# Optimization experiments

Measured on AMD Instinct MI355X. Metric: run time of the kernel, lower is better.

## Reference

```python
import jax, jax.numpy as jnp
import numpy as np

B, T, H, L = 256, 1024, 64, 5  # batch, seq_len, hidden_size, num_layers


def setup_inputs() -> dict:
    key = jax.random.key(0)
    ks = jax.random.split(key, 10)
    s = 1.0 / np.sqrt(H)  # PyTorch LSTM/Linear uniform init bound

    def u(k, shape):
        return jax.random.uniform(k, shape, jnp.float32, -s, s)

    return {
        "x": jax.random.normal(ks[0], (B, T, 1), jnp.float32),
        "w_ih0": u(ks[1], (4 * H, 1)),          # layer 0 input weights (input_size=1)
        "w_ih_rest": u(ks[2], (L - 1, 4 * H, H)),  # layers 1..4 input weights
        "w_hh": u(ks[3], (L, 4 * H, H)),
        "b_ih": u(ks[4], (L, 4 * H)),
        "b_hh": u(ks[5], (L, 4 * H)),
        "W1": u(ks[6], (H, H)),
        "b1": u(ks[7], (H,)),
        "W2": u(ks[8], (1, H)),
        "b2": u(ks[9], (1,)),
        "future": 0,
    }


def _lstm_layer(x, w_ih, w_hh, b_ih, b_hh):
    # x: [B, T, in]; PyTorch gate order i, f, g, o
    gx = jnp.einsum('bti,gi->btg', x, w_ih) + b_ih  # precompute input projections [B,T,4H]
    h0 = jnp.zeros((x.shape[0], w_hh.shape[1]), x.dtype)

    def step(carry, gxt):
        h, c = carry
        gates = gxt + h @ w_hh.T + b_hh  # [B,4H]
        i, f, g, o = jnp.split(gates, 4, axis=-1)
        c = jax.nn.sigmoid(f) * c + jax.nn.sigmoid(i) * jnp.tanh(g)
        h = jax.nn.sigmoid(o) * jnp.tanh(c)
        return (h, c), h

    _, hs = jax.lax.scan(step, (h0, h0), jnp.swapaxes(gx, 0, 1))  # scan over time
    return jnp.swapaxes(hs, 0, 1)  # [B,T,H]


def _model(x, w_ih0, w_ih_rest, w_hh, b_ih, b_hh, W1, b1, W2, b2):
    # 5-layer LSTM (inter-layer dropout=0.1 is inactive in eval mode)
    h = _lstm_layer(x, w_ih0, w_hh[0], b_ih[0], b_hh[0])
    for l in range(1, w_hh.shape[0]):
        h = _lstm_layer(h, w_ih_rest[l - 1], w_hh[l], b_ih[l], b_hh[l])
    h = jax.nn.relu(h)
    h = jax.nn.relu(h @ W1.T + b1)
    return h @ W2.T + b2  # [B,T,1]


def reference(x, w_ih0, w_ih_rest, w_hh, b_ih, b_hh, W1, b1, W2, b2, future):
    out = None
    for _ in range(future + 1):
        out = _model(x, w_ih0, w_ih_rest, w_hh, b_ih, b_hh, W1, b1, W2, b2)
        x = jnp.concatenate([x, out[:, -1:, :]], axis=1)
    return out
```

## Files before the change

kernel.cpp:

```cpp
#include <hip/hip_runtime.h>

#define B_ 256
#define T_ 1024
#define H_ 64

typedef float f32x2 __attribute__((ext_vector_type(2)));
typedef float f32x4 __attribute__((ext_vector_type(4)));

__device__ __forceinline__ float fast_sigmoid(float x) {
    float e = __builtin_amdgcn_exp2f(-1.4426950408889634f * x);
    return __builtin_amdgcn_rcpf(1.0f + e);
}
__device__ __forceinline__ float fast_tanh(float x) {
    float e = __builtin_amdgcn_exp2f(2.8853900817779268f * x);
    return 1.0f - 2.0f * __builtin_amdgcn_rcpf(1.0f + e);
}

template<int CTRL>
__device__ __forceinline__ float dpp_addf(float v) {
    int vi = __builtin_bit_cast(int, v);
    int sh = __builtin_amdgcn_update_dpp(0, vi, CTRL, 0xF, 0xF, true);
    return v + __builtin_bit_cast(float, sh);
}

__device__ __forceinline__ f32x2 lo4(f32x4 v) { return __builtin_shufflevector(v, v, 0, 1); }
__device__ __forceinline__ f32x2 hi4(f32x4 v) { return __builtin_shufflevector(v, v, 2, 3); }

__device__ __forceinline__ void block_sync_lds() {
    asm volatile("s_waitcnt lgkmcnt(0)\n\ts_barrier" ::: "memory");
}

__device__ __forceinline__ float hsum4(f32x4 v) {
    return (v.x + v.y) + (v.z + v.w);
}

__device__ __forceinline__ void dot4x16(const f32x4 wt[4][4],
                                        f32x4 h0, f32x4 h1, f32x4 h2, f32x4 h3,
                                        float acc[4]) {
    #pragma unroll
    for (int r = 0; r < 4; ++r) {
        f32x2 a = {0.f, 0.f}, d = {0.f, 0.f};
        a = __builtin_elementwise_fma(lo4(wt[r][0]), lo4(h0), a);
        d = __builtin_elementwise_fma(hi4(wt[r][0]), hi4(h0), d);
        a = __builtin_elementwise_fma(lo4(wt[r][1]), lo4(h1), a);
        d = __builtin_elementwise_fma(hi4(wt[r][1]), hi4(h1), d);
        a = __builtin_elementwise_fma(lo4(wt[r][2]), lo4(h2), a);
        d = __builtin_elementwise_fma(hi4(wt[r][2]), hi4(h2), d);
        a = __builtin_elementwise_fma(lo4(wt[r][3]), lo4(h3), a);
        d = __builtin_elementwise_fma(hi4(wt[r][3]), hi4(h3), d);
        f32x2 s = a + d;
        acc[r] = s.x + s.y;
    }
}

__global__ __attribute__((amdgpu_flat_work_group_size(768, 768)))
void lstm_pair01(const float* __restrict__ xA,
                 float* __restrict__ hB_out,
                 const float* __restrict__ wA_ih,
                 const float* __restrict__ wA_hh,
                 const float* __restrict__ bA_ih,
                 const float* __restrict__ bA_hh,
                 const float* __restrict__ wB_ih,
                 const float* __restrict__ wB_hh,
                 const float* __restrict__ bB_ih,
                 const float* __restrict__ bB_hh)
{
    const int b   = blockIdx.x;
    const int tid = threadIdx.x;
    const bool isB = (tid < 512);

    __shared__ __align__(16) float xhA[2][80];
    __shared__ __align__(16) float xhB[2][160];

    int kc, j;
    f32x4 wt[4][4];
    float bias0 = 0.f, bias1 = 0.f, bias2 = 0.f, bias3 = 0.f;
    float w00 = 0.f, w01 = 0.f, w02 = 0.f, w03 = 0.f;

    if (isB) {
        kc = tid & 7; j = tid >> 3;
        #pragma unroll
        for (int r = 0; r < 4; ++r) {
            const int row = r * H_ + j;
            const float* base = (kc < 4) ? (wB_ih + row * H_ + kc * 16)
                                         : (wB_hh + row * H_ + (kc - 4) * 16);
            #pragma unroll
            for (int q = 0; q < 4; ++q) wt[r][q] = *(const f32x4*)(base + 4 * q);
        }
        if (kc == 0) {
            bias0 = bB_ih[0*H_+j] + bB_hh[0*H_+j];
            bias1 = bB_ih[1*H_+j] + bB_hh[1*H_+j];
            bias2 = bB_ih[2*H_+j] + bB_hh[2*H_+j];
            bias3 = bB_ih[3*H_+j] + bB_hh[3*H_+j];
        }
    } else {
        const int t2 = tid - 512;
        kc = t2 & 3; j = t2 >> 2;
        #pragma unroll
        for (int r = 0; r < 4; ++r) {
            const int row = r * H_ + j;
            const float* base = wA_hh + row * H_ + kc * 16;
            #pragma unroll
            for (int q = 0; q < 4; ++q) wt[r][q] = *(const f32x4*)(base + 4 * q);
        }
        if (kc == 0) {
            bias0 = bA_ih[0*H_+j] + bA_hh[0*H_+j];
            bias1 = bA_ih[1*H_+j] + bA_hh[1*H_+j];
            bias2 = bA_ih[2*H_+j] + bA_hh[2*H_+j];
            bias3 = bA_ih[3*H_+j] + bA_hh[3*H_+j];
            w00 = wA_ih[0*H_+j]; w01 = wA_ih[1*H_+j];
            w02 = wA_ih[2*H_+j]; w03 = wA_ih[3*H_+j];
        }
    }
    #pragma unroll
    for (int r = 0; r < 4; ++r)
        #pragma unroll
        for (int q = 0; q < 4; ++q)
            asm volatile("" : "+v"(wt[r][q]));

    float c_st = 0.f;
    float xt = (!isB) ? xA[(long)b * T_] : 0.f;

    if (isB) {
        if (tid < H_) xhB[1][80 + (tid >> 4) * 20 + (tid & 15)] = 0.f;
    } else {
        const int t2 = tid - 512;
        if (t2 < H_) xhA[0][(t2 >> 4) * 20 + (t2 & 15)] = 0.f;
    }
    block_sync_lds();

    for (int s = 0; s <= T_; ++s) {
        const int rb = s & 1, wb = rb ^ 1;

        if (isB) {
            if (s >= 1) {
                const f32x4* xv = (const f32x4*)&xhB[rb][kc * 20];
                f32x4 h0 = xv[0], h1 = xv[1], h2 = xv[2], h3 = xv[3];
                float acc[4];
                dot4x16(wt, h0, h1, h2, h3, acc);
                acc[0] = dpp_addf<0xB1>(acc[0]); acc[1] = dpp_addf<0xB1>(acc[1]);
                acc[2] = dpp_addf<0xB1>(acc[2]); acc[3] = dpp_addf<0xB1>(acc[3]);
                acc[0] = dpp_addf<0x4E>(acc[0]); acc[1] = dpp_addf<0x4E>(acc[1]);
                acc[2] = dpp_addf<0x4E>(acc[2]); acc[3] = dpp_addf<0x4E>(acc[3]);
                acc[0] = dpp_addf<0x141>(acc[0]); acc[1] = dpp_addf<0x141>(acc[1]);
                acc[2] = dpp_addf<0x141>(acc[2]); acc[3] = dpp_addf<0x141>(acc[3]);
                if (kc == 0) {
                    float i_ = fast_sigmoid(acc[0] + bias0);
                    float f_ = fast_sigmoid(acc[1] + bias1);
                    float g_ = fast_tanh   (acc[2] + bias2);
                    float o_ = fast_sigmoid(acc[3] + bias3);
                    c_st = f_ * c_st + i_ * g_;
                    float h = o_ * fast_tanh(c_st);
                    xhB[wb][80 + (j >> 4) * 20 + (j & 15)] = h;
                    hB_out[((long)b * T_ + (s - 1)) * H_ + j] = h;
                }
            }
        } else {
            if (s < T_) {
                float xn = 0.f;
                if (s + 1 < T_) xn = xA[(long)b * T_ + s + 1];
                const f32x4* xv = (const f32x4*)&xhA[rb][kc * 20];
                f32x4 h0 = xv[0], h1 = xv[1], h2 = xv[2], h3 = xv[3];
                float acc[4];
                dot4x16(wt, h0, h1, h2, h3, acc);
                acc[0] = dpp_addf<0xB1>(acc[0]); acc[1] = dpp_addf<0xB1>(acc[1]);
                acc[2] = dpp_addf<0xB1>(acc[2]); acc[3] = dpp_addf<0xB1>(acc[3]);
                acc[0] = dpp_addf<0x4E>(acc[0]); acc[1] = dpp_addf<0x4E>(acc[1]);
                acc[2] = dpp_addf<0x4E>(acc[2]); acc[3] = dpp_addf<0x4E>(acc[3]);
                if (kc == 0) {
                    float gi = acc[0] + bias0 + w00 * xt;
                    float gf = acc[1] + bias1 + w01 * xt;
                    float gg = acc[2] + bias2 + w02 * xt;
                    float go = acc[3] + bias3 + w03 * xt;
                    float i_ = fast_sigmoid(gi);
                    float f_ = fast_sigmoid(gf);
                    float g_ = fast_tanh(gg);
                    float o_ = fast_sigmoid(go);
                    c_st = f_ * c_st + i_ * g_;
                    float h = o_ * fast_tanh(c_st);
                    const int off = (j >> 4) * 20 + (j & 15);
                    xhA[wb][off] = h;
                    xhB[wb][off] = h;
                }
                xt = xn;
            }
        }
        block_sync_lds();
    }
}

__global__ __attribute__((amdgpu_flat_work_group_size(768, 768)))
void lstm_triple(const float* xin,
                 float* hout,
                 const float* __restrict__ wP_ih, const float* __restrict__ wP_hh,
                 const float* __restrict__ bP_ih, const float* __restrict__ bP_hh,
                 const float* __restrict__ wM_ih, const float* __restrict__ wM_hh,
                 const float* __restrict__ bM_ih, const float* __restrict__ bM_hh,
                 const float* __restrict__ wZ_ih, const float* __restrict__ wZ_hh,
                 const float* __restrict__ bZ_ih, const float* __restrict__ bZ_hh)
{
    const int b    = blockIdx.x;
    const int tid  = threadIdx.x;
    const int role = tid >> 8;
    const int loc  = tid & 255;
    const int kc   = loc & 3;
    const int j    = loc >> 2;

    __shared__ __align__(16) float bufP[2][144];
    __shared__ __align__(16) float bufM[2][144];
    __shared__ __align__(16) float bufZ[2][144];

    const float* w_ih = (role == 0) ? wP_ih : (role == 1) ? wM_ih : wZ_ih;
    const float* w_hh = (role == 0) ? wP_hh : (role == 1) ? wM_hh : wZ_hh;
    const float* b_ih = (role == 0) ? bP_ih : (role == 1) ? bM_ih : bZ_ih;
    const float* b_hh = (role == 0) ? bP_hh : (role == 1) ? bM_hh : bZ_hh;
    float (*myBuf)[144] = (role == 0) ? bufP : (role == 1) ? bufM : bufZ;
    float (*dnBuf)[144] = (role == 0) ? bufM : (role == 1) ? bufZ : bufP;

    f32x4 wt[4][8];
    #pragma unroll
    for (int r = 0; r < 4; ++r) {
        const int row = r * H_ + j;
        const float* base = (kc < 2) ? (w_ih + row * H_ + kc * 32)
                                     : (w_hh + row * H_ + (kc - 2) * 32);
        #pragma unroll
        for (int q = 0; q < 8; ++q)
            wt[r][q] = *(const f32x4*)(base + 4 * q);
    }
    #pragma unroll
    for (int r = 0; r < 4; ++r)
        #pragma unroll
        for (int q = 0; q < 8; ++q)
            asm volatile("" : "+v"(wt[r][q]));

    float bias0 = 0.f, bias1 = 0.f, bias2 = 0.f, bias3 = 0.f;
    if (kc == 0) {
        bias0 = b_ih[0*H_+j] + b_hh[0*H_+j];
        bias1 = b_ih[1*H_+j] + b_hh[1*H_+j];
        bias2 = b_ih[2*H_+j] + b_hh[2*H_+j];
        bias3 = b_ih[3*H_+j] + b_hh[3*H_+j];
    }
    float c_st = 0.f;

    if (tid < 64) {
        const int u = tid;
        bufP[0][(u >> 5) * 36 + (u & 31)] = xin[(long)b * T_ * H_ + u];
        bufP[0][((u >> 5) + 2) * 36 + (u & 31)] = 0.f;
    } else if (tid < 128) {
        const int u = tid - 64;
        bufM[1][((u >> 5) + 2) * 36 + (u & 31)] = 0.f;
    } else if (tid < 192) {
        const int u = tid - 128;
        bufZ[0][((u >> 5) + 2) * 36 + (u & 31)] = 0.f;
    }
    block_sync_lds();

    for (int s = 0; s <= T_ + 1; ++s) {
        const int rb = s & 1, wb = rb ^ 1;
        const bool active = (role == 0) ? (s < T_)
                          : (role == 1) ? (s >= 1 && s <= T_)
                                        : (s >= 2);
        if (active) {
            float xn = 0.f;
            if (role == 0 && kc == 1 && s + 1 < T_)
                xn = xin[((long)b * T_ + s + 1) * H_ + j];

            const f32x4* xv = (const f32x4*)&myBuf[rb][kc * 36];
            f32x4 a0 = {0,0,0,0}, a1 = {0,0,0,0}, a2 = {0,0,0,0}, a3 = {0,0,0,0};
            #pragma unroll
            for (int q = 0; q < 8; ++q) {
                f32x4 hq = xv[q];
                a0 = __builtin_elementwise_fma(wt[0][q], hq, a0);
                a1 = __builtin_elementwise_fma(wt[1][q], hq, a1);
                a2 = __builtin_elementwise_fma(wt[2][q], hq, a2);
                a3 = __builtin_elementwise_fma(wt[3][q], hq, a3);
            }
            float acc0 = hsum4(a0), acc1 = hsum4(a1);
            float acc2 = hsum4(a2), acc3 = hsum4(a3);

            acc0 = dpp_addf<0xB1>(acc0); acc1 = dpp_addf<0xB1>(acc1);
            acc2 = dpp_addf<0xB1>(acc2); acc3 = dpp_addf<0xB1>(acc3);
            acc0 = dpp_addf<0x4E>(acc0); acc1 = dpp_addf<0x4E>(acc1);
            acc2 = dpp_addf<0x4E>(acc2); acc3 = dpp_addf<0x4E>(acc3);

            if (kc == 0) {
                float i_ = fast_sigmoid(acc0 + bias0);
                float f_ = fast_sigmoid(acc1 + bias1);
                float g_ = fast_tanh   (acc2 + bias2);
                float o_ = fast_sigmoid(acc3 + bias3);
                c_st = f_ * c_st + i_ * g_;
                float h = o_ * fast_tanh(c_st);
                const int hoff = ((j >> 5) + 2) * 36 + (j & 31);
                const int xoff = (j >> 5) * 36 + (j & 31);
                myBuf[wb][hoff] = h;
                if (role < 2) dnBuf[wb][xoff] = h;
                else          hout[((long)b * T_ + (s - 2)) * H_ + j] = h;
            }
            if (role == 0 && kc == 1)
                bufP[wb][(j >> 5) * 36 + (j & 31)] = xn;
        }
        block_sync_lds();
    }
}

__global__ __launch_bounds__(256)
void mlp_head_v2(const float* __restrict__ hbuf,
                 const float* __restrict__ W1,
                 const float* __restrict__ b1,
                 const float* __restrict__ W2,
                 const float* __restrict__ b2,
                 float* __restrict__ out)
{
    const long r = (long)blockIdx.x * 256 + threadIdx.x;

    float row[H_];
    const float4* src = (const float4*)(hbuf + r * H_);
    #pragma unroll
    for (int q = 0; q < 16; ++q) {
        float4 v = src[q];
        row[4*q+0] = fmaxf(v.x, 0.f); row[4*q+1] = fmaxf(v.y, 0.f);
        row[4*q+2] = fmaxf(v.z, 0.f); row[4*q+3] = fmaxf(v.w, 0.f);
    }
    #pragma unroll
    for (int q = 0; q < 16; ++q)
        asm volatile("" : "+v"(row[4*q]), "+v"(row[4*q+1]),
                         "+v"(row[4*q+2]), "+v"(row[4*q+3]));

    float acc = b2[0];
    for (int jj = 0; jj < H_; ++jj) {
        const float* wrow = W1 + jj * H_;
        float s0 = 0.f, s1 = 0.f, s2 = 0.f, s3 = 0.f;
        #pragma unroll
        for (int q = 0; q < 16; ++q) {
            s0 += row[4*q+0] * wrow[4*q+0];
            s1 += row[4*q+1] * wrow[4*q+1];
            s2 += row[4*q+2] * wrow[4*q+2];
            s3 += row[4*q+3] * wrow[4*q+3];
        }
        float y = fmaxf(b1[jj] + (s0 + s1) + (s2 + s3), 0.f);
        acc += y * W2[jj];
    }
    out[r] = acc;
}

extern "C" void kernel_launch(void* const* d_in, const int* in_sizes, int n_in,
                              void* d_out, int out_size, void* d_ws, size_t ws_size,
                              hipStream_t stream) {
    const float* x     = (const float*)d_in[0];
    const float* w_ih0 = (const float*)d_in[1];
    const float* w_ihr = (const float*)d_in[2];
    const float* w_hh  = (const float*)d_in[3];
    const float* b_ih  = (const float*)d_in[4];
    const float* b_hh  = (const float*)d_in[5];
    const float* W1    = (const float*)d_in[6];
    const float* b1    = (const float*)d_in[7];
    const float* W2    = (const float*)d_in[8];
    const float* b2    = (const float*)d_in[9];

    float* out = (float*)d_out;
    float* buf = (float*)d_ws;

    const long LW = 4L * H_ * H_;
    const long LB = 4L * H_;

    lstm_pair01<<<dim3(B_), dim3(768), 0, stream>>>(
        x, buf,
        w_ih0,          w_hh + 0 * LW, b_ih + 0 * LB, b_hh + 0 * LB,
        w_ihr + 0 * LW, w_hh + 1 * LW, b_ih + 1 * LB, b_hh + 1 * LB);

    lstm_triple<<<dim3(B_), dim3(768), 0, stream>>>(
        buf, buf,
        w_ihr + 1 * LW, w_hh + 2 * LW, b_ih + 2 * LB, b_hh + 2 * LB,
        w_ihr + 2 * LW, w_hh + 3 * LW, b_ih + 3 * LB, b_hh + 3 * LB,
        w_ihr + 3 * LW, w_hh + 4 * LW, b_ih + 4 * LB, b_hh + 4 * LB);

    mlp_head_v2<<<dim3((B_ * T_) / 256), dim3(256), 0, stream>>>(
        buf, W1, b1, W2, b2, out);
}
```

Measured before the change: 1.752 ms.

## Overlap LSTM layer pair and triple in one kernel via global flags

Merges the two LSTM kernels into one launch of 512 blocks. The first 256 blocks run layers 0-1, and the other 256 run layers 2-4 while spinning on per-8-timestep flags in global memory, so the two stages pipeline instead of running back to back. The flags live in the tail of the output buffer and rely on all 512 blocks being co-resident (256 CUs, one 768-thread block each may fit two per CU). It adds atomic stores, threadfences and spin-waits, and risks deadlock if the consumer blocks are scheduled before the producers. Stale magic values left in the output tail from a previous call could also let consumers run ahead of the producers.

```diff
diff --git a/kernel.cpp b/kernel.cpp
--- a/kernel.cpp
+++ b/kernel.cpp
@@ -3,6 +3,7 @@
 #define B_ 256
 #define T_ 1024
 #define H_ 64
+#define MAGIC_ 0x5EED7A61u
 
 typedef float f32x2 __attribute__((ext_vector_type(2)));
 typedef float f32x4 __attribute__((ext_vector_type(4)));
@@ -23,283 +24,321 @@
     return v + __builtin_bit_cast(float, sh);
 }
 
-__device__ __forceinline__ f32x2 lo4(f32x4 v) { return __builtin_shufflevector(v, v, 0, 1); }
-__device__ __forceinline__ f32x2 hi4(f32x4 v) { return __builtin_shufflevector(v, v, 2, 3); }
-
 __device__ __forceinline__ void block_sync_lds() {
     asm volatile("s_waitcnt lgkmcnt(0)\n\ts_barrier" ::: "memory");
 }
 
-__device__ __forceinline__ float hsum4(f32x4 v) {
-    return (v.x + v.y) + (v.z + v.w);
-}
-
-__device__ __forceinline__ void dot4x16(const f32x4 wt[4][4],
-                                        f32x4 h0, f32x4 h1, f32x4 h2, f32x4 h3,
-                                        float acc[4]) {
-    #pragma unroll
-    for (int r = 0; r < 4; ++r) {
-        f32x2 a = {0.f, 0.f}, d = {0.f, 0.f};
-        a = __builtin_elementwise_fma(lo4(wt[r][0]), lo4(h0), a);
-        d = __builtin_elementwise_fma(hi4(wt[r][0]), hi4(h0), d);
-        a = __builtin_elementwise_fma(lo4(wt[r][1]), lo4(h1), a);
-        d = __builtin_elementwise_fma(hi4(wt[r][1]), hi4(h1), d);
-        a = __builtin_elementwise_fma(lo4(wt[r][2]), lo4(h2), a);
-        d = __builtin_elementwise_fma(hi4(wt[r][2]), hi4(h2), d);
-        a = __builtin_elementwise_fma(lo4(wt[r][3]), lo4(h3), a);
-        d = __builtin_elementwise_fma(hi4(wt[r][3]), hi4(h3), d);
-        f32x2 s = a + d;
-        acc[r] = s.x + s.y;
-    }
+__device__ __forceinline__ float hsum4(f32x4 v) { return (v.x + v.y) + (v.z + v.w); }
+
+__device__ __forceinline__ void spin_flag(const unsigned* f) {
+    while (__hip_atomic_load(f, __ATOMIC_RELAXED, __HIP_MEMORY_SCOPE_AGENT) != MAGIC_)
+        __builtin_amdgcn_s_sleep(2);
 }
 
 __global__ __attribute__((amdgpu_flat_work_group_size(768, 768)))
-void lstm_pair01(const float* __restrict__ xA,
-                 float* __restrict__ hB_out,
-                 const float* __restrict__ wA_ih,
-                 const float* __restrict__ wA_hh,
-                 const float* __restrict__ bA_ih,
-                 const float* __restrict__ bA_hh,
-                 const float* __restrict__ wB_ih,
-                 const float* __restrict__ wB_hh,
-                 const float* __restrict__ bB_ih,
-                 const float* __restrict__ bB_hh)
+void lstm_overlap(const float* __restrict__ x,
+                  float* buf,
+                  unsigned* __restrict__ flags,
+                  const float* __restrict__ w_ih0,
+                  const float* __restrict__ w_ihr,
+                  const float* __restrict__ w_hh,
+                  const float* __restrict__ b_ih,
+                  const float* __restrict__ b_hh)
 {
-    const int b   = blockIdx.x;
-    const int tid = threadIdx.x;
-    const bool isB = (tid < 512);
+    const int brole = blockIdx.x >> 8;
+    const int b     = blockIdx.x & 255;
+    const int tid   = threadIdx.x;
 
     __shared__ __align__(16) float xhA[2][80];
     __shared__ __align__(16) float xhB[2][160];
-
-    int kc, j;
-    f32x4 wt[4][4];
-    float bias0 = 0.f, bias1 = 0.f, bias2 = 0.f, bias3 = 0.f;
-    float w00 = 0.f, w01 = 0.f, w02 = 0.f, w03 = 0.f;
-
-    if (isB) {
-        kc = tid & 7; j = tid >> 3;
+    __shared__ __align__(16) float bufP[2][144];
+    __shared__ __align__(16) float bufM[2][144];
+    __shared__ __align__(16) float bufZ[2][144];
+
+    f32x4 wt[4][8];
+
+    const long LW = 4L * H_ * H_;
+    const long LB = 4L * H_;
+
+    if (brole == 0) {
+        const float* wA_ih = w_ih0;
+        const float* wA_hh = w_hh;
+        const float* bA_ih = b_ih;            const float* bA_hh = b_hh;
+        const float* wB_ih = w_ihr;
+        const float* wB_hh = w_hh + LW;
+        const float* bB_ih = b_ih + LB;       const float* bB_hh = b_hh + LB;
+        float* hB_out = buf;
+
+        const bool isB = (tid < 512);
+        int kc, j;
+        float bias0 = 0.f, bias1 = 0.f, bias2 = 0.f, bias3 = 0.f;
+        float w00 = 0.f, w01 = 0.f, w02 = 0.f, w03 = 0.f;
+
+        if (isB) {
+            kc = tid & 7; j = tid >> 3;
+            #pragma unroll
+            for (int r = 0; r < 4; ++r) {
+                const int row = r * H_ + j;
+                const float* base = (kc < 4) ? (wB_ih + row * H_ + kc * 16)
+                                             : (wB_hh + row * H_ + (kc - 4) * 16);
+                #pragma unroll
+                for (int q = 0; q < 4; ++q) wt[r][q] = *(const f32x4*)(base + 4 * q);
+            }
+            if (kc == 0) {
+                bias0 = bB_ih[0*H_+j] + bB_hh[0*H_+j];
+                bias1 = bB_ih[1*H_+j] + bB_hh[1*H_+j];
+                bias2 = bB_ih[2*H_+j] + bB_hh[2*H_+j];
+                bias3 = bB_ih[3*H_+j] + bB_hh[3*H_+j];
+            }
+        } else {
+            const int t2 = tid - 512;
+            kc = t2 & 3; j = t2 >> 2;
+            #pragma unroll
+            for (int r = 0; r < 4; ++r) {
+                const int row = r * H_ + j;
+                const float* base = wA_hh + row * H_ + kc * 16;
+                #pragma unroll
+                for (int q = 0; q < 4; ++q) wt[r][q] = *(const f32x4*)(base + 4 * q);
+            }
+            if (kc == 0) {
+                bias0 = bA_ih[0*H_+j] + bA_hh[0*H_+j];
+                bias1 = bA_ih[1*H_+j] + bA_hh[1*H_+j];
+                bias2 = bA_ih[2*H_+j] + bA_hh[2*H_+j];
+                bias3 = bA_ih[3*H_+j] + bA_hh[3*H_+j];
+                w00 = wA_ih[0*H_+j]; w01 = wA_ih[1*H_+j];
+                w02 = wA_ih[2*H_+j]; w03 = wA_ih[3*H_+j];
+            }
+        }
+        #pragma unroll
+        for (int r = 0; r < 4; ++r)
+            #pragma unroll
+            for (int q = 0; q < 4; ++q)
+                asm volatile("" : "+v"(wt[r][q]));
+
+        float c_st = 0.f;
+        float xt = (!isB) ? x[(long)b * T_] : 0.f;
+
+        if (isB) {
+            if (tid < H_) xhB[1][80 + (tid >> 4) * 20 + (tid & 15)] = 0.f;
+        } else {
+            const int t2 = tid - 512;
+            if (t2 < H_) xhA[0][(t2 >> 4) * 20 + (t2 & 15)] = 0.f;
+        }
+        block_sync_lds();
+
+        for (int s = 0; s <= T_; ++s) {
+            const int rb = s & 1, wb = rb ^ 1;
+
+            if (isB) {
+                if (s >= 1) {
+                    const f32x4* xv = (const f32x4*)&xhB[rb][kc * 20];
+                    f32x4 h0 = xv[0], h1 = xv[1], h2 = xv[2], h3 = xv[3];
+                    f32x4 a0 = {0,0,0,0}, a1 = {0,0,0,0}, a2 = {0,0,0,0}, a3 = {0,0,0,0};
+                    a0 = __builtin_elementwise_fma(wt[0][0], h0, a0);
+                    a1 = __builtin_elementwise_fma(wt[1][0], h0, a1);
+                    a2 = __builtin_elementwise_fma(wt[2][0], h0, a2);
+                    a3 = __builtin_elementwise_fma(wt[3][0], h0, a3);
+                    a0 = __builtin_elementwise_fma(wt[0][1], h1, a0);
+                    a1 = __builtin_elementwise_fma(wt[1][1], h1, a1);
+                    a2 = __builtin_elementwise_fma(wt[2][1], h1, a2);
+                    a3 = __builtin_elementwise_fma(wt[3][1], h1, a3);
+                    a0 = __builtin_elementwise_fma(wt[0][2], h2, a0);
+                    a1 = __builtin_elementwise_fma(wt[1][2], h2, a1);
+                    a2 = __builtin_elementwise_fma(wt[2][2], h2, a2);
+                    a3 = __builtin_elementwise_fma(wt[3][2], h2, a3);
+                    a0 = __builtin_elementwise_fma(wt[0][3], h3, a0);
+                    a1 = __builtin_elementwise_fma(wt[1][3], h3, a1);
+                    a2 = __builtin_elementwise_fma(wt[2][3], h3, a2);
+                    a3 = __builtin_elementwise_fma(wt[3][3], h3, a3);
+                    float acc0 = hsum4(a0), acc1 = hsum4(a1);
+                    float acc2 = hsum4(a2), acc3 = hsum4(a3);
+                    acc0 = dpp_addf<0xB1>(acc0); acc1 = dpp_addf<0xB1>(acc1);
+                    acc2 = dpp_addf<0xB1>(acc2); acc3 = dpp_addf<0xB1>(acc3);
+                    acc0 = dpp_addf<0x4E>(acc0); acc1 = dpp_addf<0x4E>(acc1);
+                    acc2 = dpp_addf<0x4E>(acc2); acc3 = dpp_addf<0x4E>(acc3);
+                    acc0 = dpp_addf<0x141>(acc0); acc1 = dpp_addf<0x141>(acc1);
+                    acc2 = dpp_addf<0x141>(acc2); acc3 = dpp_addf<0x141>(acc3);
+                    if (kc == 0) {
+                        float i_ = fast_sigmoid(acc0 + bias0);
+                        float f_ = fast_sigmoid(acc1 + bias1);
+                        float g_ = fast_tanh   (acc2 + bias2);
+                        float o_ = fast_sigmoid(acc3 + bias3);
+                        c_st = f_ * c_st + i_ * g_;
+                        float h = o_ * fast_tanh(c_st);
+                        xhB[wb][80 + (j >> 4) * 20 + (j & 15)] = h;
+                        __hip_atomic_store(&hB_out[((long)b * T_ + (s - 1)) * H_ + j],
+                                           h, __ATOMIC_RELAXED, __HIP_MEMORY_SCOPE_AGENT);
+                    }
+                }
+            } else {
+                if (s < T_) {
+                    float xn = 0.f;
+                    if (s + 1 < T_) xn = x[(long)b * T_ + s + 1];
+                    const f32x4* xv = (const f32x4*)&xhA[rb][kc * 20];
+                    f32x4 h0 = xv[0], h1 = xv[1], h2 = xv[2], h3 = xv[3];
+                    f32x4 a0 = {0,0,0,0}, a1 = {0,0,0,0}, a2 = {0,0,0,0}, a3 = {0,0,0,0};
+                    a0 = __builtin_elementwise_fma(wt[0][0], h0, a0);
+                    a1 = __builtin_elementwise_fma(wt[1][0], h0, a1);
+                    a2 = __builtin_elementwise_fma(wt[2][0], h0, a2);
+                    a3 = __builtin_elementwise_fma(wt[3][0], h0, a3);
+                    a0 = __builtin_elementwise_fma(wt[0][1], h1, a0);
+                    a1 = __builtin_elementwise_fma(wt[1][1], h1, a1);
+                    a2 = __builtin_elementwise_fma(wt[2][1], h1, a2);
+                    a3 = __builtin_elementwise_fma(wt[3][1], h1, a3);
+                    a0 = __builtin_elementwise_fma(wt[0][2], h2, a0);
+                    a1 = __builtin_elementwise_fma(wt[1][2], h2, a1);
+                    a2 = __builtin_elementwise_fma(wt[2][2], h2, a2);
+                    a3 = __builtin_elementwise_fma(wt[3][2], h2, a3);
+                    a0 = __builtin_elementwise_fma(wt[0][3], h3, a0);
+                    a1 = __builtin_elementwise_fma(wt[1][3], h3, a1);
+                    a2 = __builtin_elementwise_fma(wt[2][3], h3, a2);
+                    a3 = __builtin_elementwise_fma(wt[3][3], h3, a3);
+                    float acc0 = hsum4(a0), acc1 = hsum4(a1);
+                    float acc2 = hsum4(a2), acc3 = hsum4(a3);
+                    acc0 = dpp_addf<0xB1>(acc0); acc1 = dpp_addf<0xB1>(acc1);
+                    acc2 = dpp_addf<0xB1>(acc2); acc3 = dpp_addf<0xB1>(acc3);
+                    acc0 = dpp_addf<0x4E>(acc0); acc1 = dpp_addf<0x4E>(acc1);
+                    acc2 = dpp_addf<0x4E>(acc2); acc3 = dpp_addf<0x4E>(acc3);
+                    if (kc == 0) {
+                        float i_ = fast_sigmoid(acc0 + bias0 + w00 * xt);
+                        float f_ = fast_sigmoid(acc1 + bias1 + w01 * xt);
+                        float g_ = fast_tanh   (acc2 + bias2 + w02 * xt);
+                        float o_ = fast_sigmoid(acc3 + bias3 + w03 * xt);
+                        c_st = f_ * c_st + i_ * g_;
+                        float h = o_ * fast_tanh(c_st);
+                        const int off = (j >> 4) * 20 + (j & 15);
+                        xhA[wb][off] = h;
+                        xhB[wb][off] = h;
+                    }
+                    xt = xn;
+                }
+            }
+            block_sync_lds();
+
+            const int trow = s - 1;
+            if (trow >= 0 && (trow & 7) == 7) {
+                __threadfence();
+                block_sync_lds();
+                if (tid == 0)
+                    __hip_atomic_store(&flags[b * 128 + (trow >> 3)], MAGIC_,
+                                       __ATOMIC_RELAXED, __HIP_MEMORY_SCOPE_AGENT);
+            }
+        }
+    } else {
+        const float* xin  = buf;
+        float*       hout = buf;
+        const float* wP_ih = w_ihr + 1 * LW;  const float* wP_hh = w_hh + 2 * LW;
+        const float* bP_ih = b_ih + 2 * LB;   const float* bP_hh = b_hh + 2 * LB;
+        const float* wM_ih = w_ihr + 2 * LW;  const float* wM_hh = w_hh + 3 * LW;
+        const float* bM_ih = b_ih + 3 * LB;   const float* bM_hh = b_hh + 3 * LB;
+        const float* wZ_ih = w_ihr + 3 * LW;  const float* wZ_hh = w_hh + 4 * LW;
+        const float* bZ_ih = b_ih + 4 * LB;   const float* bZ_hh = b_hh + 4 * LB;
+
+        const int role = tid >> 8;
+        const int loc  = tid & 255;
+        const int kc   = loc & 3;
+        const int j    = loc >> 2;
+
+        const float* w_ih = (role == 0) ? wP_ih : (role == 1) ? wM_ih : wZ_ih;
+        const float* w_hh2 = (role == 0) ? wP_hh : (role == 1) ? wM_hh : wZ_hh;
+        const float* b_ih2 = (role == 0) ? bP_ih : (role == 1) ? bM_ih : bZ_ih;
+        const float* b_hh2 = (role == 0) ? bP_hh : (role == 1) ? bM_hh : bZ_hh;
+        float (*myBuf)[144] = (role == 0) ? bufP : (role == 1) ? bufM : bufZ;
+        float (*dnBuf)[144] = (role == 0) ? bufM : (role == 1) ? bufZ : bufP;
+
         #pragma unroll
         for (int r = 0; r < 4; ++r) {
             const int row = r * H_ + j;
-            const float* base = (kc < 4) ? (wB_ih + row * H_ + kc * 16)
-                                         : (wB_hh + row * H_ + (kc - 4) * 16);
+            const float* base = (kc < 2) ? (w_ih + row * H_ + kc * 32)
+                                         : (w_hh2 + row * H_ + (kc - 2) * 32);
             #pragma unroll
-            for (int q = 0; q < 4; ++q) wt[r][q] = *(const f32x4*)(base + 4 * q);
-        }
+            for (int q = 0; q < 8; ++q)
+                wt[r][q] = *(const f32x4*)(base + 4 * q);
+        }
+        #pragma unroll
+        for (int r = 0; r < 4; ++r)
+            #pragma unroll
+            for (int q = 0; q < 8; ++q)
+                asm volatile("" : "+v"(wt[r][q]));
+
+        float bias0 = 0.f, bias1 = 0.f, bias2 = 0.f, bias3 = 0.f;
         if (kc == 0) {
-            bias0 = bB_ih[0*H_+j] + bB_hh[0*H_+j];
-            bias1 = bB_ih[1*H_+j] + bB_hh[1*H_+j];
-            bias2 = bB_ih[2*H_+j] + bB_hh[2*H_+j];
-            bias3 = bB_ih[3*H_+j] + bB_hh[3*H_+j];
-        }
-    } else {
-        const int t2 = tid - 512;
-        kc = t2 & 3; j = t2 >> 2;
-        #pragma unroll
-        for (int r = 0; r < 4; ++r) {
-            const int row = r * H_ + j;
-            const float* base = wA_hh + row * H_ + kc * 16;
-            #pragma unroll
-            for (int q = 0; q < 4; ++q) wt[r][q] = *(const f32x4*)(base + 4 * q);
-        }
-        if (kc == 0) {
-            bias0 = bA_ih[0*H_+j] + bA_hh[0*H_+j];
-            bias1 = bA_ih[1*H_+j] + bA_hh[1*H_+j];
-            bias2 = bA_ih[2*H_+j] + bA_hh[2*H_+j];
-            bias3 = bA_ih[3*H_+j] + bA_hh[3*H_+j];
-            w00 = wA_ih[0*H_+j]; w01 = wA_ih[1*H_+j];
-            w02 = wA_ih[2*H_+j]; w03 = wA_ih[3*H_+j];
-        }
-    }
-    #pragma unroll
-    for (int r = 0; r < 4; ++r)
-        #pragma unroll
-        for (int q = 0; q < 4; ++q)
-            asm volatile("" : "+v"(wt[r][q]));
-
-    float c_st = 0.f;
-    float xt = (!isB) ? xA[(long)b * T_] : 0.f;
-
-    if (isB) {
-        if (tid < H_) xhB[1][80 + (tid >> 4) * 20 + (tid & 15)] = 0.f;
-    } else {
-        const int t2 = tid - 512;
-        if (t2 < H_) xhA[0][(t2 >> 4) * 20 + (t2 & 15)] = 0.f;
-    }
-    block_sync_lds();
-
-    for (int s = 0; s <= T_; ++s) {
-        const int rb = s & 1, wb = rb ^ 1;
-
-        if (isB) {
-            if (s >= 1) {
-                const f32x4* xv = (const f32x4*)&xhB[rb][kc * 20];
-                f32x4 h0 = xv[0], h1 = xv[1], h2 = xv[2], h3 = xv[3];
-                float acc[4];
-                dot4x16(wt, h0, h1, h2, h3, acc);
-                acc[0] = dpp_addf<0xB1>(acc[0]); acc[1] = dpp_addf<0xB1>(acc[1]);
-                acc[2] = dpp_addf<0xB1>(acc[2]); acc[3] = dpp_addf<0xB1>(acc[3]);
-                acc[0] = dpp_addf<0x4E>(acc[0]); acc[1] = dpp_addf<0x4E>(acc[1]);
-                acc[2] = dpp_addf<0x4E>(acc[2]); acc[3] = dpp_addf<0x4E>(acc[3]);
-                acc[0] = dpp_addf<0x141>(acc[0]); acc[1] = dpp_addf<0x141>(acc[1]);
-                acc[2] = dpp_addf<0x141>(acc[2]); acc[3] = dpp_addf<0x141>(acc[3]);
+            bias0 = b_ih2[0*H_+j] + b_hh2[0*H_+j];
+            bias1 = b_ih2[1*H_+j] + b_hh2[1*H_+j];
+            bias2 = b_ih2[2*H_+j] + b_hh2[2*H_+j];
+            bias3 = b_ih2[3*H_+j] + b_hh2[3*H_+j];
+        }
+        float c_st = 0.f;
+
+        if (tid == 0) spin_flag(&flags[b * 128]);
+        block_sync_lds();
+
+        if (tid < H_) {
+            const int u = tid;
+            bufP[0][(u >> 5) * 36 + (u & 31)] =
+                __hip_atomic_load(&xin[(long)b * T_ * H_ + u],
+                                  __ATOMIC_RELAXED, __HIP_MEMORY_SCOPE_AGENT);
+            bufP[0][((u >> 5) + 2) * 36 + (u & 31)] = 0.f;
+        } else if (tid < 128) {
+            const int u = tid - 64;
+            bufM[1][((u >> 5) + 2) * 36 + (u & 31)] = 0.f;
+        } else if (tid < 192) {
+            const int u = tid - 128;
+            bufZ[0][((u >> 5) + 2) * 36 + (u & 31)] = 0.f;
+        }
+        block_sync_lds();
+
+        for (int s = 0; s <= T_ + 1; ++s) {
+            if (((s + 1) & 7) == 0 && (s + 1) < T_) {
+                if (tid == 0) spin_flag(&flags[b * 128 + ((s + 1) >> 3)]);
+                block_sync_lds();
+            }
+
+            const int rb = s & 1, wb = rb ^ 1;
+            const bool active = (role == 0) ? (s < T_)
+                              : (role == 1) ? (s >= 1 && s <= T_)
+                                            : (s >= 2);
+            if (active) {
+                float xn = 0.f;
+                if (role == 0 && kc == 1 && s + 1 < T_)
+                    xn = __hip_atomic_load(&xin[((long)b * T_ + s + 1) * H_ + j],
+                                           __ATOMIC_RELAXED, __HIP_MEMORY_SCOPE_AGENT);
+
+                const f32x4* xv = (const f32x4*)&myBuf[rb][kc * 36];
+                f32x4 a0 = {0,0,0,0}, a1 = {0,0,0,0}, a2 = {0,0,0,0}, a3 = {0,0,0,0};
+                #pragma unroll
+                for (int q = 0; q < 8; ++q) {
+                    f32x4 hq = xv[q];
+                    a0 = __builtin_elementwise_fma(wt[0][q], hq, a0);
+                    a1 = __builtin_elementwise_fma(wt[1][q], hq, a1);
+                    a2 = __builtin_elementwise_fma(wt[2][q], hq, a2);
+                    a3 = __builtin_elementwise_fma(wt[3][q], hq, a3);
+                }
+                float acc0 = hsum4(a0), acc1 = hsum4(a1);
+                float acc2 = hsum4(a2), acc3 = hsum4(a3);
+                acc0 = dpp_addf<0xB1>(acc0); acc1 = dpp_addf<0xB1>(acc1);
+                acc2 = dpp_addf<0xB1>(acc2); acc3 = dpp_addf<0xB1>(acc3);
+                acc0 = dpp_addf<0x4E>(acc0); acc1 = dpp_addf<0x4E>(acc1);
+                acc2 = dpp_addf<0x4E>(acc2); acc3 = dpp_addf<0x4E>(acc3);
+
                 if (kc == 0) {
-                    float i_ = fast_sigmoid(acc[0] + bias0);
-                    float f_ = fast_sigmoid(acc[1] + bias1);
-                    float g_ = fast_tanh   (acc[2] + bias2);
-                    float o_ = fast_sigmoid(acc[3] + bias3);
+                    float i_ = fast_sigmoid(acc0 + bias0);
+                    float f_ = fast_sigmoid(acc1 + bias1);
+                    float g_ = fast_tanh   (acc2 + bias2);
+                    float o_ = fast_sigmoid(acc3 + bias3);
                     c_st = f_ * c_st + i_ * g_;
                     float h = o_ * fast_tanh(c_st);
-                    xhB[wb][80 + (j >> 4) * 20 + (j & 15)] = h;
-                    hB_out[((long)b * T_ + (s - 1)) * H_ + j] = h;
+                    myBuf[wb][((j >> 5) + 2) * 36 + (j & 31)] = h;
+                    if (role < 2)
+                        dnBuf[wb][(j >> 5) * 36 + (j & 31)] = h;
+                    else
+                        hout[((long)b * T_ + (s - 2)) * H_ + j] = h;
                 }
-            }
-        } else {
-            if (s < T_) {
-                float xn = 0.f;
-                if (s + 1 < T_) xn = xA[(long)b * T_ + s + 1];
-                const f32x4* xv = (const f32x4*)&xhA[rb][kc * 20];
-                f32x4 h0 = xv[0], h1 = xv[1], h2 = xv[2], h3 = xv[3];
-                float acc[4];
-                dot4x16(wt, h0, h1, h2, h3, acc);
-                acc[0] = dpp_addf<0xB1>(acc[0]); acc[1] = dpp_addf<0xB1>(acc[1]);
-                acc[2] = dpp_addf<0xB1>(acc[2]); acc[3] = dpp_addf<0xB1>(acc[3]);
-                acc[0] = dpp_addf<0x4E>(acc[0]); acc[1] = dpp_addf<0x4E>(acc[1]);
-                acc[2] = dpp_addf<0x4E>(acc[2]); acc[3] = dpp_addf<0x4E>(acc[3]);
-                if (kc == 0) {
-                    float gi = acc[0] + bias0 + w00 * xt;
-                    float gf = acc[1] + bias1 + w01 * xt;
-                    float gg = acc[2] + bias2 + w02 * xt;
-                    float go = acc[3] + bias3 + w03 * xt;
-                    float i_ = fast_sigmoid(gi);
-                    float f_ = fast_sigmoid(gf);
-                    float g_ = fast_tanh(gg);
-                    float o_ = fast_sigmoid(go);
-                    c_st = f_ * c_st + i_ * g_;
-                    float h = o_ * fast_tanh(c_st);
-                    const int off = (j >> 4) * 20 + (j & 15);
-                    xhA[wb][off] = h;
-                    xhB[wb][off] = h;
-                }
-                xt = xn;
-            }
-        }
-        block_sync_lds();
-    }
-}
-
-__global__ __attribute__((amdgpu_flat_work_group_size(768, 768)))
-void lstm_triple(const float* xin,
-                 float* hout,
-                 const float* __restrict__ wP_ih, const float* __restrict__ wP_hh,
-                 const float* __restrict__ bP_ih, const float* __restrict__ bP_hh,
-                 const float* __restrict__ wM_ih, const float* __restrict__ wM_hh,
-                 const float* __restrict__ bM_ih, const float* __restrict__ bM_hh,
-                 const float* __restrict__ wZ_ih, const float* __restrict__ wZ_hh,
-                 const float* __restrict__ bZ_ih, const float* __restrict__ bZ_hh)
-{
-    const int b    = blockIdx.x;
-    const int tid  = threadIdx.x;
-    const int role = tid >> 8;
-    const int loc  = tid & 255;
-    const int kc   = loc & 3;
-    const int j    = loc >> 2;
-
-    __shared__ __align__(16) float bufP[2][144];
-    __shared__ __align__(16) float bufM[2][144];
-    __shared__ __align__(16) float bufZ[2][144];
-
-    const float* w_ih = (role == 0) ? wP_ih : (role == 1) ? wM_ih : wZ_ih;
-    const float* w_hh = (role == 0) ? wP_hh : (role == 1) ? wM_hh : wZ_hh;
-    const float* b_ih = (role == 0) ? bP_ih : (role == 1) ? bM_ih : bZ_ih;
-    const float* b_hh = (role == 0) ? bP_hh : (role == 1) ? bM_hh : bZ_hh;
-    float (*myBuf)[144] = (role == 0) ? bufP : (role == 1) ? bufM : bufZ;
-    float (*dnBuf)[144] = (role == 0) ? bufM : (role == 1) ? bufZ : bufP;
-
-    f32x4 wt[4][8];
-    #pragma unroll
-    for (int r = 0; r < 4; ++r) {
-        const int row = r * H_ + j;
-        const float* base = (kc < 2) ? (w_ih + row * H_ + kc * 32)
-                                     : (w_hh + row * H_ + (kc - 2) * 32);
-        #pragma unroll
-        for (int q = 0; q < 8; ++q)
-            wt[r][q] = *(const f32x4*)(base + 4 * q);
-    }
-    #pragma unroll
-    for (int r = 0; r < 4; ++r)
-        #pragma unroll
-        for (int q = 0; q < 8; ++q)
-            asm volatile("" : "+v"(wt[r][q]));
-
-    float bias0 = 0.f, bias1 = 0.f, bias2 = 0.f, bias3 = 0.f;
-    if (kc == 0) {
-        bias0 = b_ih[0*H_+j] + b_hh[0*H_+j];
-        bias1 = b_ih[1*H_+j] + b_hh[1*H_+j];
-        bias2 = b_ih[2*H_+j] + b_hh[2*H_+j];
-        bias3 = b_ih[3*H_+j] + b_hh[3*H_+j];
-    }
-    float c_st = 0.f;
-
-    if (tid < 64) {
-        const int u = tid;
-        bufP[0][(u >> 5) * 36 + (u & 31)] = xin[(long)b * T_ * H_ + u];
-        bufP[0][((u >> 5) + 2) * 36 + (u & 31)] = 0.f;
-    } else if (tid < 128) {
-        const int u = tid - 64;
-        bufM[1][((u >> 5) + 2) * 36 + (u & 31)] = 0.f;
-    } else if (tid < 192) {
-        const int u = tid - 128;
-        bufZ[0][((u >> 5) + 2) * 36 + (u & 31)] = 0.f;
-    }
-    block_sync_lds();
-
-    for (int s = 0; s <= T_ + 1; ++s) {
-        const int rb = s & 1, wb = rb ^ 1;
-        const bool active = (role == 0) ? (s < T_)
-                          : (role == 1) ? (s >= 1 && s <= T_)
-                                        : (s >= 2);
-        if (active) {
-            float xn = 0.f;
-            if (role == 0 && kc == 1 && s + 1 < T_)
-                xn = xin[((long)b * T_ + s + 1) * H_ + j];
-
-            const f32x4* xv = (const f32x4*)&myBuf[rb][kc * 36];
-            f32x4 a0 = {0,0,0,0}, a1 = {0,0,0,0}, a2 = {0,0,0,0}, a3 = {0,0,0,0};
-            #pragma unroll
-            for (int q = 0; q < 8; ++q) {
-                f32x4 hq = xv[q];
-                a0 = __builtin_elementwise_fma(wt[0][q], hq, a0);
-                a1 = __builtin_elementwise_fma(wt[1][q], hq, a1);
-                a2 = __builtin_elementwise_fma(wt[2][q], hq, a2);
-                a3 = __builtin_elementwise_fma(wt[3][q], hq, a3);
-            }
-            float acc0 = hsum4(a0), acc1 = hsum4(a1);
-            float acc2 = hsum4(a2), acc3 = hsum4(a3);
-
-            acc0 = dpp_addf<0xB1>(acc0); acc1 = dpp_addf<0xB1>(acc1);
-            acc2 = dpp_addf<0xB1>(acc2); acc3 = dpp_addf<0xB1>(acc3);
-            acc0 = dpp_addf<0x4E>(acc0); acc1 = dpp_addf<0x4E>(acc1);
-            acc2 = dpp_addf<0x4E>(acc2); acc3 = dpp_addf<0x4E>(acc3);
-
-            if (kc == 0) {
-                float i_ = fast_sigmoid(acc0 + bias0);
-                float f_ = fast_sigmoid(acc1 + bias1);
-                float g_ = fast_tanh   (acc2 + bias2);
-                float o_ = fast_sigmoid(acc3 + bias3);
-                c_st = f_ * c_st + i_ * g_;
-                float h = o_ * fast_tanh(c_st);
-                const int hoff = ((j >> 5) + 2) * 36 + (j & 31);
-                const int xoff = (j >> 5) * 36 + (j & 31);
-                myBuf[wb][hoff] = h;
-                if (role < 2) dnBuf[wb][xoff] = h;
-                else          hout[((long)b * T_ + (s - 2)) * H_ + j] = h;
-            }
-            if (role == 0 && kc == 1)
-                bufP[wb][(j >> 5) * 36 + (j & 31)] = xn;
-        }
-        block_sync_lds();
+                if (role == 0 && kc == 1)
+                    bufP[wb][(j >> 5) * 36 + (j & 31)] = xn;
+            }
+            block_sync_lds();
+        }
     }
 }
 
@@ -360,19 +399,10 @@
     float* out = (float*)d_out;
     float* buf = (float*)d_ws;
 
-    const long LW = 4L * H_ * H_;
-    const long LB = 4L * H_;
-
-    lstm_pair01<<<dim3(B_), dim3(768), 0, stream>>>(
-        x, buf,
-        w_ih0,          w_hh + 0 * LW, b_ih + 0 * LB, b_hh + 0 * LB,
-        w_ihr + 0 * LW, w_hh + 1 * LW, b_ih + 1 * LB, b_hh + 1 * LB);
-
-    lstm_triple<<<dim3(B_), dim3(768), 0, stream>>>(
-        buf, buf,
-        w_ihr + 1 * LW, w_hh + 2 * LW, b_ih + 2 * LB, b_hh + 2 * LB,
-        w_ihr + 2 * LW, w_hh + 3 * LW, b_ih + 3 * LB, b_hh + 3 * LB,
-        w_ihr + 3 * LW, w_hh + 4 * LW, b_ih + 4 * LB, b_hh + 4 * LB);
+    unsigned* flags = (unsigned*)(out + (out_size - 32768));
+
+    lstm_overlap<<<dim3(512), dim3(768), 0, stream>>>(
+        x, buf, flags, w_ih0, w_ihr, w_hh, b_ih, b_hh);
 
     mlp_head_v2<<<dim3((B_ * T_) / 256), dim3(256), 0, stream>>>(
         buf, W1, b1, W2, b2, out);
```

Result: slower. 6.867 ms (+292.0%).
